# Optimization experiments

Hardware: AMD Instinct MI355X
Metric: run time of the kernel (lower is better)

Reference implementation:

```python
import jax, jax.numpy as jnp
import numpy as np
import math

B, H, L, DK, D, LOCAL = 4, 8, 2048, 64, 512, 4


def setup_inputs() -> dict:
    key = jax.random.key(0)
    ks = jax.random.split(key, 9)
    n = L
    return {
        'query': jax.random.normal(ks[0], (B, H, L, DK), jnp.float32),
        'key': jax.random.normal(ks[1], (B, H, L, DK), jnp.float32),
        'value': jax.random.normal(ks[2], (B, H, L, DK), jnp.float32),
        'users': jax.random.normal(ks[3], (B, L, D), jnp.float32),
        'mask': jnp.tril(jnp.ones((L, L), dtype=bool))[None, None],  # causal [1,1,L,L]
        'rel_pos_w': jax.random.normal(ks[4], (2 * n - 1, DK * LOCAL), jnp.float32) * 0.02,
        'user_proj_w': jax.random.normal(ks[5], (DK * LOCAL, D), jnp.float32) * 0.02,
        'user_proj_b': jax.random.normal(ks[6], (DK * LOCAL,), jnp.float32) * 0.02,
        'mlp_w': jax.random.normal(ks[7], (LOCAL, DK), jnp.float32) * 0.1,
        'mlp_b': jax.random.normal(ks[8], (LOCAL,), jnp.float32) * 0.1,
    }


def reference(query, key, value, users, mask, rel_pos_w, user_proj_w, user_proj_b, mlp_w, mlp_b):
    b, h, l, dk = query.shape
    local = mlp_w.shape[0]
    g = h - local
    n = l
    scale = 1.0 / math.sqrt(dk)
    NEG = -1e12  # MAX_VAL in the torch source

    # ---- global heads: plain softmax attention ----
    qg, kg, vg = query[:, :g], key[:, :g], value[:, :g]
    sg = jnp.einsum('bhqd,bhkd->bhqk', qg, kg) * scale
    sg = jnp.where(mask, sg, NEG)
    pg = jax.nn.softmax(sg, axis=-1)
    og = jnp.einsum('bhqk,bhkd->bhqd', pg, vg)

    # ---- local (LOCKER) heads ----
    ql, kl, vl = query[:, g:], key[:, g:], value[:, g:]
    sl = jnp.einsum('bhqd,bhkd->bhqk', ql, kl) * scale

    # reweight = Linear(d_k,1)(rel_pos + v_q + v_k + user_proj(users)_q) per local head.
    # Linear over a sum decomposes exactly (same math, avoids [b,local,l,l,dk] tensor):
    rel_tab = rel_pos_w.reshape(2 * n - 1, local, dk)
    rel_scores = jnp.einsum('rhd,hd->rh', rel_tab, mlp_w)          # [2n-1, local]
    pos = jnp.arange(n)
    distance = pos[None, :] - pos[:, None] + n - 1                  # [l, l]
    rel_term = rel_scores[distance].transpose(2, 0, 1)              # [local, l, l]

    v_term = jnp.einsum('bhkd,hd->bhk', vl, mlp_w)                  # [b, local, l]
    u = (users @ user_proj_w.T + user_proj_b).reshape(b, l, local, dk)
    u_term = jnp.einsum('bqhd,hd->bhq', u, mlp_w)                   # [b, local, l]

    reweight = (rel_term[None]
                + v_term[:, :, None, :]      # value_l.unsqueeze(-3): varies over key idx
                + v_term[:, :, :, None]      # value_l.unsqueeze(-2): varies over query idx
                + u_term[:, :, :, None]      # user term broadcast over key idx
                + mlp_b[None, :, None, None])

    sl = sl + reweight
    sl = jnp.where(mask, sl, NEG)
    pl = jax.nn.softmax(sl, axis=-1)
    ol = jnp.einsum('bhqk,bhkd->bhqd', pl, vl)

    return jnp.concatenate([og, ol], axis=1)  # [b, h, l, d_k]
```

## Files before the change

kernel.cpp:

```cpp
#include <hip/hip_runtime.h>

#define TL 2048
#define NHEAD 8
#define NLOC 4
#define L2E 1.44269504f

typedef __attribute__((ext_vector_type(4))) float f32x4;
typedef __attribute__((ext_vector_type(8))) __bf16 bf16x8;
typedef __attribute__((ext_vector_type(8))) unsigned short u16x8;

static __device__ __forceinline__ unsigned short f2bf(float f) {
    unsigned u = __float_as_uint(f);
    u = (u + 0x7FFFu + ((u >> 16) & 1u)) >> 16;
    return (unsigned short)u;
}
static __device__ __forceinline__ float bf2f(unsigned short u) {
    return __uint_as_float(((unsigned)u) << 16);
}
static __device__ __forceinline__ void gl_lds16(const void* g, void* l) {
    __builtin_amdgcn_global_load_lds(
        (const __attribute__((address_space(1))) void*)g,
        (__attribute__((address_space(3))) void*)l, 16, 0, 0);
}

__global__ __launch_bounds__(256) void relscore_kernel(
    const float* __restrict__ rel_pos_w, const float* __restrict__ mlp_w,
    unsigned short* __restrict__ rel_sb) {
    int r = blockIdx.x;
    int t = threadIdx.x;
    int w = t >> 6, lane = t & 63;
    float v = rel_pos_w[r * 256 + t] * mlp_w[t];
#pragma unroll
    for (int off = 32; off; off >>= 1) v += __shfl_xor(v, off);
    if (lane == 0) rel_sb[w * 4096 + r] = f2bf(v * L2E);
}

__global__ __launch_bounds__(256) void vterm_kernel(
    const float* __restrict__ value, const float* __restrict__ mlp_w,
    unsigned short* __restrict__ vtb) {
    int t = threadIdx.x;
    int lane = t & 63;
    int w = blockIdx.x * 4 + (t >> 6);
    int k = w & (TL - 1);
    int hp = (w >> 11) & 3;
    int b = w >> 13;
    float v = value[((size_t)((b * NHEAD + NLOC + hp) * TL + k) << 6) + lane] *
              mlp_w[hp * 64 + lane];
#pragma unroll
    for (int off = 32; off; off >>= 1) v += __shfl_xor(v, off);
    if (lane == 0) vtb[w] = f2bf(v * L2E);
}

__global__ __launch_bounds__(256) void preconv_kernel(
    const float* __restrict__ key, const float* __restrict__ value,
    unsigned short* __restrict__ Kb, unsigned short* __restrict__ Vtb) {
    __shared__ float Vf[64][66];
    int blk = blockIdx.x;
    int t = threadIdx.x;
    size_t src = (size_t)blk * 4096;
    size_t dst = (size_t)blk * 4096;

#pragma unroll
    for (int i = 0; i < 2; ++i) {
        int ch = t + i * 256;
        int row = ch >> 3, c = ch & 7;
        const float* kp = key + src + row * 64 + c * 8;
        f32x4 a = *(const f32x4*)kp;
        f32x4 bb = *(const f32x4*)(kp + 4);
        u16x8 o;
#pragma unroll
        for (int j = 0; j < 4; ++j) { o[j] = f2bf(a[j]); o[4 + j] = f2bf(bb[j]); }
        *(u16x8*)&Kb[dst + row * 64 + ((c ^ (row & 7)) << 3)] = o;
    }
    {
        int row = t >> 2, q4 = t & 3;
        const float* vp = value + src + row * 64 + q4 * 16;
#pragma unroll
        for (int j = 0; j < 4; ++j)
            *(f32x4*)&Vf[row][q4 * 16 + j * 4] = *(const f32x4*)(vp + j * 4);
    }
    __syncthreads();
#pragma unroll
    for (int i = 0; i < 2; ++i) {
        int ch = t + i * 256;
        int dr = ch >> 3, c = ch & 7;
        u16x8 o;
#pragma unroll
        for (int j = 0; j < 8; ++j) o[j] = f2bf(Vf[c * 8 + j][dr]);
        *(u16x8*)&Vtb[dst + dr * 64 + ((c ^ (dr & 7)) << 3)] = o;
    }
}

__global__ __launch_bounds__(256, 4) void attn_kernel(
    const float* __restrict__ query,
    const unsigned short* __restrict__ Kb, const unsigned short* __restrict__ Vtb,
    const unsigned short* __restrict__ rel_sb, const unsigned short* __restrict__ vtb,
    float* __restrict__ out) {

    __shared__ __align__(16) unsigned char smem[37248];
    unsigned short* Ks0  = (unsigned short*)smem;
    unsigned short* Vt0  = (unsigned short*)(smem + 16384);
    unsigned short* relb = (unsigned short*)(smem + 32768);
    unsigned short* bias0 = (unsigned short*)(smem + 36992);

    int bid = blockIdx.x;
    int qbi = bid >> 5;
    int bh = bid & 31;
    int qb = (qbi < 16) ? (31 - qbi) : (qbi - 16);
    int h = bh & 7;
    int b = bh >> 3;
    int q0 = qb << 6;
    int t = threadIdx.x;
    int wave = t >> 6, lane = t & 63;
    int l15 = lane & 15, l4 = lane >> 4;
    bool islocal = (h >= NLOC);

    size_t base = (size_t)bh * TL * 64;
    const unsigned short* Ktiles = Kb + (size_t)bh * 32 * 4096;
    const unsigned short* Vtiles = Vtb + (size_t)bh * 32 * 4096;
    const unsigned short* vtp =
        vtb + (islocal ? (size_t)((b * NLOC + h - NLOC) * TL) : 0);

    gl_lds16(Ktiles + t * 8, Ks0 + t * 8);
    gl_lds16(Ktiles + 2048 + t * 8, Ks0 + 2048 + t * 8);
    gl_lds16(Vtiles + t * 8, Vt0 + t * 8);
    gl_lds16(Vtiles + 2048 + t * 8, Vt0 + 2048 + t * 8);
    if (islocal) {
        const u16x8* src = (const u16x8*)(rel_sb + (h - NLOC) * 4096);
        u16x8* dst = (u16x8*)relb;
        dst[t] = src[t];
        if (t < 8) {
            dst[256 + t] = src[256 + t];
            *(u16x8*)&bias0[t * 8] = *(const u16x8*)&vtp[t * 8];
        }
    }

    int qt = q0 + wave * 16;
    int q = qt + l15;

    const float SC = 0.125f * L2E;
    bf16x8 qf0, qf1;
    {
        const float* qsrc = query + base + (size_t)q * 64 + l4 * 8;
        f32x4 a = *(const f32x4*)qsrc;
        f32x4 bb = *(const f32x4*)(qsrc + 4);
        f32x4 c = *(const f32x4*)(qsrc + 32);
        f32x4 d = *(const f32x4*)(qsrc + 36);
        u16x8 u0, u1;
#pragma unroll
        for (int j = 0; j < 4; ++j) {
            u0[j] = f2bf(a[j] * SC); u0[4 + j] = f2bf(bb[j] * SC);
            u1[j] = f2bf(c[j] * SC); u1[4 + j] = f2bf(d[j] * SC);
        }
        qf0 = __builtin_bit_cast(bf16x8, u0);
        qf1 = __builtin_bit_cast(bf16x8, u1);
    }

    float m = -1e30f, lsum = 0.0f;
    f32x4 acc0 = {0.f, 0.f, 0.f, 0.f};
    f32x4 acc1 = acc0, acc2 = acc0, acc3 = acc0;

    __syncthreads();

    int cur = 0;
    for (int kt = 0; kt <= qb; ++kt) {
        unsigned short* Ks = Ks0 + cur * 4096;
        unsigned short* Vt = Vt0 + cur * 4096;
        unsigned short* bias = bias0 + cur * 64;

        if (kt < qb) {
            int nb = cur ^ 1;
            const unsigned short* gk = Ktiles + (size_t)(kt + 1) * 4096;
            const unsigned short* gv = Vtiles + (size_t)(kt + 1) * 4096;
            gl_lds16(gk + t * 8, Ks0 + nb * 4096 + t * 8);
            gl_lds16(gk + 2048 + t * 8, Ks0 + nb * 4096 + 2048 + t * 8);
            gl_lds16(gv + t * 8, Vt0 + nb * 4096 + t * 8);
            gl_lds16(gv + 2048 + t * 8, Vt0 + nb * 4096 + 2048 + t * 8);
            if (islocal && t < 8)
                *(u16x8*)&bias0[nb * 64 + t * 8] =
                    *(const u16x8*)&vtp[(kt + 1) * 64 + t * 8];
        }

        int k0 = kt << 6;
        bool diag = (kt == qb);
        int s16max = diag ? wave : 3;

        f32x4 sfr[4];
#pragma unroll
        for (int s16 = 0; s16 < 4; ++s16) {
            if (s16 <= s16max) {
                int r = s16 * 16 + l15;
                int sw = r & 7;
                const bf16x8 kf0 = *(const bf16x8*)&Ks[r * 64 + ((l4 ^ sw) << 3)];
                const bf16x8 kf1 = *(const bf16x8*)&Ks[r * 64 + (((4 + l4) ^ sw) << 3)];
                f32x4 z = {0.f, 0.f, 0.f, 0.f};
                z = __builtin_amdgcn_mfma_f32_16x16x32_bf16(kf0, qf0, z, 0, 0, 0);
                z = __builtin_amdgcn_mfma_f32_16x16x32_bf16(kf1, qf1, z, 0, 0, 0);
                sfr[s16] = z;
            } else {
                sfr[s16] = (f32x4){-1e30f, -1e30f, -1e30f, -1e30f};
            }
        }

        float sv[16];
        float tmax = -1e30f;
#pragma unroll
        for (int s16 = 0; s16 < 4; ++s16) {
#pragma unroll
            for (int rg = 0; rg < 4; ++rg) {
                int kk = s16 * 16 + l4 * 4 + rg;
                int k = k0 + kk;
                float s = sfr[s16][rg];
                if (s16 <= s16max) {
                    if (islocal) s += bf2f(relb[k - q + 2047]) + bf2f(bias[kk]);
                    if (diag && k > q) s = -1e30f;
                }
                sv[s16 * 4 + rg] = s;
                tmax = fmaxf(tmax, s);
            }
        }
        tmax = fmaxf(tmax, __shfl_xor(tmax, 16));
        tmax = fmaxf(tmax, __shfl_xor(tmax, 32));
        float newm = fmaxf(m, tmax);
        float corr = exp2f(m - newm);
        float psum = 0.f;
        unsigned short pu[16];
#pragma unroll
        for (int i = 0; i < 16; ++i) {
            float p = exp2f(sv[i] - newm);
            psum += p;
            pu[i] = f2bf(p);
        }
        psum += __shfl_xor(psum, 16);
        psum += __shfl_xor(psum, 32);
        lsum = lsum * corr + psum;
        m = newm;
        acc0 *= corr; acc1 *= corr; acc2 *= corr; acc3 *= corr;

        __syncthreads();

        unsigned short* Pw = Ks + wave * 1024;
#pragma unroll
        for (int s16 = 0; s16 < 4; ++s16) {
            unsigned long long pk =
                (unsigned long long)pu[s16 * 4 + 0] |
                ((unsigned long long)pu[s16 * 4 + 1] << 16) |
                ((unsigned long long)pu[s16 * 4 + 2] << 32) |
                ((unsigned long long)pu[s16 * 4 + 3] << 48);
            int c = 2 * s16 + (l4 >> 1);
            Pw[l15 * 64 + ((c ^ (l15 & 7)) << 3) + ((l4 & 1) << 2)] = 0;
            *(unsigned long long*)&Pw[l15 * 64 + ((c ^ (l15 & 7)) << 3) + ((l4 & 1) << 2)] = pk;
        }

#pragma unroll
        for (int half = 0; half < 2; ++half) {
            const bf16x8 pf =
                *(const bf16x8*)&Pw[l15 * 64 + (((half * 4 + l4) ^ (l15 & 7)) << 3)];
            int cbase = half * 4 + l4;
#pragma unroll
            for (int dblk = 0; dblk < 4; ++dblk) {
                int r = dblk * 16 + l15;
                const bf16x8 vf =
                    *(const bf16x8*)&Vt[r * 64 + ((cbase ^ (r & 7)) << 3)];
                f32x4* ac = dblk == 0 ? &acc0 : dblk == 1 ? &acc1
                          : dblk == 2 ? &acc2 : &acc3;
                *ac = __builtin_amdgcn_mfma_f32_16x16x32_bf16(vf, pf, *ac, 0, 0, 0);
            }
        }

        __syncthreads();
        cur ^= 1;
    }

    float invl = 1.0f / lsum;
    float* ob = (float*)(smem + wave * 4352);
    *(f32x4*)&ob[l15 * 68 + 0  + l4 * 4] = acc0 * invl;
    *(f32x4*)&ob[l15 * 68 + 16 + l4 * 4] = acc1 * invl;
    *(f32x4*)&ob[l15 * 68 + 32 + l4 * 4] = acc2 * invl;
    *(f32x4*)&ob[l15 * 68 + 48 + l4 * 4] = acc3 * invl;
    size_t obase = base + (size_t)qt * 64;
#pragma unroll
    for (int it = 0; it < 4; ++it) {
        int row = lane >> 2;
        int col = (lane & 3) * 16 + it * 4;
        f32x4 o = *(const f32x4*)&ob[row * 68 + col];
        *(f32x4*)(out + obase + (size_t)row * 64 + col) = o;
    }
}

extern "C" void kernel_launch(void* const* d_in, const int* in_sizes, int n_in,
                              void* d_out, int out_size, void* d_ws, size_t ws_size,
                              hipStream_t stream) {
    const float* query = (const float*)d_in[0];
    const float* key = (const float*)d_in[1];
    const float* value = (const float*)d_in[2];
    const float* rel_pos_w = (const float*)d_in[5];
    const float* mlp_w = (const float*)d_in[8];
    float* out = (float*)d_out;

    unsigned short* Kb = (unsigned short*)d_ws;
    unsigned short* Vtb = Kb + 32 * 32 * 4096;
    unsigned short* rel_sb = Vtb + 32 * 32 * 4096;
    unsigned short* vtb = rel_sb + 4 * 4096;

    relscore_kernel<<<4095, 256, 0, stream>>>(rel_pos_w, mlp_w, rel_sb);
    vterm_kernel<<<8192, 256, 0, stream>>>(value, mlp_w, vtb);
    preconv_kernel<<<1024, 256, 0, stream>>>(key, value, Kb, Vtb);
    attn_kernel<<<1024, 256, 0, stream>>>(query, Kb, Vtb, rel_sb, vtb, out);
}
```

Before: 92.24 us.

## Fuse v-term into preconv, add lazy softmax rescale, streamline P store

Drops the separate vterm kernel launch and computes the local-head value projection inside preconv from the V tile already staged in shared memory, so value is not read a second time. In the attention loop the running max and accumulator rescale are updated only when some lane's tile max exceeds the current max by a threshold (lazy rescaling). The redundant zero store is removed and the P tile is packed with native bf16 conversion. The full __syncthreads is replaced by an explicit lgkmcnt wait, s_barrier and sched_barrier. Lazy rescaling lets exp2 arguments reach up to about 2^11.5 before a rescale, which relies on the float32 accumulators and lsum having enough headroom.

Measured after the change: 88.95 us. -3.6%, faster.

```diff
diff --git a/kernel.cpp b/kernel.cpp
--- a/kernel.cpp
+++ b/kernel.cpp
@@ -7,6 +7,7 @@
 
 typedef __attribute__((ext_vector_type(4))) float f32x4;
 typedef __attribute__((ext_vector_type(8))) __bf16 bf16x8;
+typedef __attribute__((ext_vector_type(4))) __bf16 bf16x4;
 typedef __attribute__((ext_vector_type(8))) unsigned short u16x8;
 
 static __device__ __forceinline__ unsigned short f2bf(float f) {
@@ -35,28 +36,16 @@
     if (lane == 0) rel_sb[w * 4096 + r] = f2bf(v * L2E);
 }
 
-__global__ __launch_bounds__(256) void vterm_kernel(
-    const float* __restrict__ value, const float* __restrict__ mlp_w,
-    unsigned short* __restrict__ vtb) {
-    int t = threadIdx.x;
-    int lane = t & 63;
-    int w = blockIdx.x * 4 + (t >> 6);
-    int k = w & (TL - 1);
-    int hp = (w >> 11) & 3;
-    int b = w >> 13;
-    float v = value[((size_t)((b * NHEAD + NLOC + hp) * TL + k) << 6) + lane] *
-              mlp_w[hp * 64 + lane];
-#pragma unroll
-    for (int off = 32; off; off >>= 1) v += __shfl_xor(v, off);
-    if (lane == 0) vtb[w] = f2bf(v * L2E);
-}
-
 __global__ __launch_bounds__(256) void preconv_kernel(
     const float* __restrict__ key, const float* __restrict__ value,
-    unsigned short* __restrict__ Kb, unsigned short* __restrict__ Vtb) {
+    const float* __restrict__ mlp_w,
+    unsigned short* __restrict__ Kb, unsigned short* __restrict__ Vtb,
+    unsigned short* __restrict__ vtb) {
     __shared__ float Vf[64][66];
     int blk = blockIdx.x;
     int t = threadIdx.x;
+    int bh = blk >> 5, kt = blk & 31;
+    int h = bh & 7, b = bh >> 3;
     size_t src = (size_t)blk * 4096;
     size_t dst = (size_t)blk * 4096;
 
@@ -88,6 +77,19 @@
 #pragma unroll
         for (int j = 0; j < 8; ++j) o[j] = f2bf(Vf[c * 8 + j][dr]);
         *(u16x8*)&Vtb[dst + dr * 64 + ((c ^ (dr & 7)) << 3)] = o;
+    }
+    if (h >= NLOC) {
+        int wave = t >> 6, lane = t & 63;
+        float mw = mlp_w[(h - NLOC) * 64 + lane];
+        unsigned short* vout = vtb + (size_t)((b * NLOC + h - NLOC) * TL) + kt * 64;
+#pragma unroll
+        for (int i = 0; i < 16; ++i) {
+            int row = wave * 16 + i;
+            float v = Vf[row][lane] * mw;
+#pragma unroll
+            for (int off = 32; off; off >>= 1) v += __shfl_xor(v, off);
+            if (lane == 0) vout[row] = f2bf(v * L2E);
+        }
     }
 }
 
@@ -221,35 +223,38 @@
         }
         tmax = fmaxf(tmax, __shfl_xor(tmax, 16));
         tmax = fmaxf(tmax, __shfl_xor(tmax, 32));
-        float newm = fmaxf(m, tmax);
-        float corr = exp2f(m - newm);
+        if (__any(tmax > m + 11.5f)) {
+            float newm = fmaxf(m, tmax);
+            float corr = exp2f(m - newm);
+            lsum *= corr;
+            acc0 *= corr; acc1 *= corr; acc2 *= corr; acc3 *= corr;
+            m = newm;
+        }
         float psum = 0.f;
-        unsigned short pu[16];
-#pragma unroll
-        for (int i = 0; i < 16; ++i) {
-            float p = exp2f(sv[i] - newm);
-            psum += p;
-            pu[i] = f2bf(p);
+        bf16x4 pq[4];
+#pragma unroll
+        for (int s16 = 0; s16 < 4; ++s16) {
+#pragma unroll
+            for (int rg = 0; rg < 4; ++rg) {
+                float p = exp2f(sv[s16 * 4 + rg] - m);
+                psum += p;
+                pq[s16][rg] = (__bf16)p;
+            }
         }
         psum += __shfl_xor(psum, 16);
         psum += __shfl_xor(psum, 32);
-        lsum = lsum * corr + psum;
-        m = newm;
-        acc0 *= corr; acc1 *= corr; acc2 *= corr; acc3 *= corr;
-
-        __syncthreads();
+        lsum += psum;
+
+        asm volatile("s_waitcnt lgkmcnt(0)" ::: "memory");
+        __builtin_amdgcn_s_barrier();
+        __builtin_amdgcn_sched_barrier(0);
 
         unsigned short* Pw = Ks + wave * 1024;
 #pragma unroll
         for (int s16 = 0; s16 < 4; ++s16) {
-            unsigned long long pk =
-                (unsigned long long)pu[s16 * 4 + 0] |
-                ((unsigned long long)pu[s16 * 4 + 1] << 16) |
-                ((unsigned long long)pu[s16 * 4 + 2] << 32) |
-                ((unsigned long long)pu[s16 * 4 + 3] << 48);
             int c = 2 * s16 + (l4 >> 1);
-            Pw[l15 * 64 + ((c ^ (l15 & 7)) << 3) + ((l4 & 1) << 2)] = 0;
-            *(unsigned long long*)&Pw[l15 * 64 + ((c ^ (l15 & 7)) << 3) + ((l4 & 1) << 2)] = pk;
+            *(unsigned long long*)&Pw[l15 * 64 + ((c ^ (l15 & 7)) << 3) + ((l4 & 1) << 2)] =
+                __builtin_bit_cast(unsigned long long, pq[s16]);
         }
 
 #pragma unroll
@@ -304,7 +309,6 @@
     unsigned short* vtb = rel_sb + 4 * 4096;
 
     relscore_kernel<<<4095, 256, 0, stream>>>(rel_pos_w, mlp_w, rel_sb);
-    vterm_kernel<<<8192, 256, 0, stream>>>(value, mlp_w, vtb);
-    preconv_kernel<<<1024, 256, 0, stream>>>(key, value, Kb, Vtb);
+    preconv_kernel<<<1024, 256, 0, stream>>>(key, value, mlp_w, Kb, Vtb, vtb);
     attn_kernel<<<1024, 256, 0, stream>>>(query, Kb, Vtb, rel_sb, vtb, out);
 }
```
